# Kernel optimization log

Hardware: AMD Instinct MI355X
Metric: run time of the kernel (lower is better)

Reference implementation:

```python
import jax, jax.numpy as jnp
import numpy as np
import math

B, H, W, Cv, Ct, T = 8, 64, 64, 256, 512, 100
TOP_M = 5
N_PAD = 8  # last N_PAD text tokens are all-zero padding


def _xavier(key, fi, fo):
    lim = math.sqrt(6.0 / (fi + fo))
    return jax.random.uniform(key, (fi, fo), jnp.float32, -lim, lim)


def layernorm(x, g, b, eps=1e-5):
    m = x.mean(-1, keepdims=True)
    v = ((x - m) ** 2).mean(-1, keepdims=True)
    return (x - m) * jax.lax.rsqrt(v + eps) * g + b


def l2norm(x, eps=1e-6):
    n = jnp.sqrt((x * x).sum(-1, keepdims=True))
    return x / jnp.maximum(n, eps)


def setup_inputs() -> dict:
    key = jax.random.key(0)
    ks = jax.random.split(key, 10)
    visual = jax.random.normal(ks[0], (B, H, W, Cv), jnp.float32)
    text = jax.random.normal(ks[1], (B, T, Ct), jnp.float32)
    text = text.at[:, T - N_PAD:, :].set(0.0)  # padded tokens
    return {
        'visual_features': visual,
        'text_features': text,
        'ln1_g': jnp.ones((Cv,), jnp.float32),
        'ln1_b': jnp.zeros((Cv,), jnp.float32),
        'qw': _xavier(ks[2], Cv, Ct), 'qb': jnp.zeros((Ct,), jnp.float32),
        'vw': _xavier(ks[3], Ct, Cv), 'vb': jnp.zeros((Cv,), jnp.float32),
        'gate_w': jax.random.normal(ks[4], (Cv, 1), jnp.float32) * 0.02,
        'gate_b': jnp.zeros((1,), jnp.float32),
        'logit_scale': jnp.asarray(math.log(1.0 / 0.07), jnp.float32),
        'alpha': jnp.asarray(0.1, jnp.float32),
        'ln2_g': jnp.ones((Cv,), jnp.float32),
        'ln2_b': jnp.zeros((Cv,), jnp.float32),
        'w1': jax.random.normal(ks[5], (Cv, 4 * Cv), jnp.float32) * 0.02,
        'b1': jnp.zeros((4 * Cv,), jnp.float32),
        'w2': jax.random.normal(ks[6], (4 * Cv, Cv), jnp.float32) * 0.02,
        'b2': jnp.zeros((Cv,), jnp.float32),
        'top_m': TOP_M,
    }


def reference(visual_features, text_features, ln1_g, ln1_b, qw, qb, vw, vb,
              gate_w, gate_b, logit_scale, alpha, ln2_g, ln2_b, w1, b1, w2, b2,
              top_m):
    Bv, Hh, Ww, C = visual_features.shape
    N = Hh * Ww
    x = layernorm(visual_features, ln1_g, ln1_b).reshape(Bv, N, C)
    q = l2norm(x @ qw + qb)                     # (B,N,Ct)
    k = l2norm(text_features)                   # (B,T,Ct)
    v = text_features @ vw + vb                 # (B,T,Cv)
    pad = jnp.abs(text_features).sum(-1) <= 1e-6  # (B,T) True = padding
    Ctd = float(qw.shape[1])
    scale = jnp.exp(jnp.clip(logit_scale, -2.0, 2.0)) / math.sqrt(Ctd)
    sim = jnp.einsum('bnc,btc->bnt', q, k) * scale
    top_vals, top_idx = jax.lax.top_k(sim, top_m)       # (B,N,M)
    pad_top = jax.vmap(lambda p, i: p[i])(pad, top_idx)  # (B,N,M)
    top_vals = jnp.where(pad_top, -jnp.inf, top_vals)
    attn = jax.nn.softmax(top_vals, axis=-1)
    v_sel = jax.vmap(lambda vb_, ib: vb_[ib])(v, top_idx)  # (B,N,M,Cv)
    aligned = jnp.einsum('bnm,bnmc->bnc', attn, v_sel)
    gate = jax.nn.sigmoid(x @ gate_w + gate_b)  # (B,N,1)
    aligned = aligned * gate
    y = x + alpha * aligned
    y = layernorm(y, ln2_g, ln2_b)
    y = y + (jax.nn.gelu(y @ w1 + b1, approximate=False) @ w2 + b2)
    return y.reshape(Bv, Hh, Ww, C)
```

## Files before the change

kernel.cpp:

```cpp
#include <hip/hip_runtime.h>
#include <hip/hip_bf16.h>
#include <math.h>

using bf16 = __hip_bfloat16;
typedef __attribute__((ext_vector_type(8))) short s16x8;
typedef __attribute__((ext_vector_type(4))) short s16x4;
typedef __attribute__((ext_vector_type(4))) float f32x4;
typedef __attribute__((ext_vector_type(4))) unsigned int u32x4;

static __device__ __forceinline__ float bits2f(unsigned short u) {
  union { unsigned int i; float f; } c; c.i = ((unsigned int)u) << 16; return c.f;
}
static __device__ __forceinline__ unsigned short f2bits(float f) {
  bf16 h = __float2bfloat16(f);
  return *reinterpret_cast<unsigned short*>(&h);
}
static __device__ __forceinline__ unsigned short scrub16(unsigned short u, unsigned short repl) {
  return ((u & 0x7F80u) == 0x7F80u) ? repl : u;
}
static __device__ __forceinline__ unsigned short f2bits_s(float f, unsigned short repl) {
  return scrub16(f2bits(f), repl);
}
static __device__ __forceinline__ float ldf_s(const float* p, float repl) {
  unsigned int w = *reinterpret_cast<const unsigned int*>(p);
  if ((w & 0x7F800000u) == 0x7F800000u) return repl;
  union { unsigned int i; float f; } c; c.i = w; return c.f;
}
static __device__ __forceinline__ float stf_s(float f, float repl) {
  union { float f; unsigned int i; } c; c.f = f;
  if ((c.i & 0x7F800000u) == 0x7F800000u) return repl;
  return f;
}
static __device__ __forceinline__ s16x8 pack8(const float* p) {
  union { f32x4 f; float fe[4]; unsigned int u[4]; } a, b;
  a.f = *reinterpret_cast<const f32x4*>(p);
  b.f = *reinterpret_cast<const f32x4*>(p + 4);
  s16x8 v;
  #pragma unroll
  for (int e = 0; e < 4; e++) {
    const float fa = ((a.u[e] & 0x7F800000u) == 0x7F800000u) ? 0.f : a.fe[e];
    const float fb = ((b.u[e] & 0x7F800000u) == 0x7F800000u) ? 0.f : b.fe[e];
    v[e]     = (short)f2bits_s(fa, 0);
    v[e + 4] = (short)f2bits_s(fb, 0);
  }
  return v;
}
static __device__ __forceinline__ float gelu_fast(float t) {
  const float u = fmaf(0.044715f * t * t, t, t);
  const float e = __expf(-1.5957691216057308f * u);
  return __fdividef(t, 1.f + e);
}
static __device__ __forceinline__ void gload_lds16(const unsigned short* g, unsigned short* l) {
  __builtin_amdgcn_global_load_lds(
      (const __attribute__((address_space(1))) void*)g,
      (__attribute__((address_space(3))) void*)l, 16, 0, 0);
}

static __device__ __forceinline__ float block_sum(float v, float* red, int tid) {
  #pragma unroll
  for (int o = 32; o > 0; o >>= 1) v += __shfl_down(v, o, 64);
  __syncthreads();
  if ((tid & 63) == 0) red[tid >> 6] = v;
  __syncthreads();
  return red[0] + red[1] + red[2] + red[3];
}

__global__ __launch_bounds__(256)
void k_preps(const float* __restrict__ qw, unsigned short* __restrict__ qwt,
             const float* __restrict__ text, unsigned short* __restrict__ khat,
             int* __restrict__ padf,
             const float* __restrict__ w1, const float* __restrict__ w2,
             unsigned short* __restrict__ w1s, unsigned short* __restrict__ w2s,
             int do_ffn,
             const float* __restrict__ vw, const float* __restrict__ vb_,
             float* __restrict__ vf) {
  __shared__ float red[4];
  __shared__ float s_t[512];
  const int bid = blockIdx.x;
  const int tid = threadIdx.x;

  if (bid < 512) {
    const int n = bid, k = tid;
    qwt[n * 256 + (k ^ ((n & 7) << 3))] = f2bits_s(ldf_s(&qw[(long)k * 512 + n], 0.f), 0);
    return;
  }
  if (bid < 1408) {
    const int j = bid - 512;
    const int t = j % 112, b = j / 112;
    unsigned short* kr = khat + ((long)b * 112 + t) * 512;
    if (t >= 100) {
      if (tid < 64) *reinterpret_cast<s16x8*>(&kr[tid * 8]) = (s16x8){0,0,0,0,0,0,0,0};
      return;
    }
    const float* tr = text + ((long)b * 100 + t) * 512;
    const float v0 = ldf_s(&tr[tid], 0.f), v1 = ldf_s(&tr[tid + 256], 0.f);
    const float ss = block_sum(fmaf(v0, v0, v1 * v1), red, tid);
    const float sa = block_sum(fabsf(v0) + fabsf(v1), red, tid);
    const float inv = 1.f / fmaxf(sqrtf(ss), 1e-6f);
    const int ks = tid ^ ((t & 7) << 3);
    kr[ks]       = f2bits_s(v0 * inv, 0);
    kr[ks + 256] = f2bits_s(v1 * inv, 0);
    if (tid == 0) padf[b * 100 + t] = (sa <= 1e-6f) ? 1 : 0;
    return;
  }
  if (bid < 3456) {
    if (!do_ffn) return;
    const int i = (bid - 1408) * 256 + tid;
    if (i < 262144) {
      const int h = i >> 8, k = i & 255;
      w1s[h * 256 + (k ^ ((h & 7) << 3))] = f2bits(w1[(long)k * 1024 + h]);
    } else {
      const int j = i - 262144;
      const int c = j >> 10, h = j & 1023;
      const int hs = (h & ~63) | ((h & 63) ^ ((c & 7) << 3));
      w2s[(long)c * 1024 + hs] = f2bits(w2[(long)h * 256 + c]);
    }
    return;
  }
  {
    const int bt = bid - 3456;
    const float* tr = text + (long)bt * 512;
    s_t[tid]       = ldf_s(&tr[tid], 0.f);
    s_t[tid + 256] = ldf_s(&tr[tid + 256], 0.f);
    __syncthreads();
    float acc = 0.f;
    for (int k = 0; k < 512; k++) acc = fmaf(s_t[k], vw[k * 256 + tid], acc);
    vf[(long)bt * 256 + tid] = stf_s(acc + vb_[tid], 0.f);
  }
}

__global__ __launch_bounds__(512)
void k_simattn(float* xv, const unsigned short* __restrict__ qwt,
               const float* __restrict__ qb, const unsigned short* __restrict__ khat,
               const float* __restrict__ ls, const float* __restrict__ ln1g,
               const float* __restrict__ ln1b, const int* __restrict__ pad,
               const float* __restrict__ v, const float* __restrict__ gate_w,
               const float* __restrict__ gate_b, const float* __restrict__ alpha,
               const float* __restrict__ ln2g, const float* __restrict__ ln2b) {
  __shared__ __align__(16) unsigned short s_q[64][520];
  __shared__ __align__(16) char s_unb[65536];
  __shared__ float s_qn[64];
  unsigned short* s_un = reinterpret_cast<unsigned short*>(s_unb);

  const int tid  = threadIdx.x;
  const int lane = tid & 63;
  const int w    = tid >> 6;
  const int l15  = lane & 15;
  const int lg   = lane >> 4;
  const int b    = blockIdx.y;
  const long grow = (long)b * 4096 + (long)blockIdx.x * 64;

  #pragma unroll
  for (int it = 0; it < 8; it++) {
    const int u = tid + it * 512;
    gload_lds16(&qwt[u * 8], &s_un[u * 8]);
  }

  const int R1 = (w >> 2) * 32;
  s16x8 xa[2][8];
  #pragma unroll
  for (int rb = 0; rb < 2; rb++) {
    float* xr = &xv[(grow + R1 + rb * 16 + l15) * 256 + lg * 8];
    float raw[8][8];
    float sm = 0.f, sq = 0.f;
    #pragma unroll
    for (int ks = 0; ks < 8; ks++) {
      union { f32x4 f; float fe[4]; unsigned int u_[4]; } a, c;
      a.f = *reinterpret_cast<const f32x4*>(xr + ks * 32);
      c.f = *reinterpret_cast<const f32x4*>(xr + ks * 32 + 4);
      #pragma unroll
      for (int e = 0; e < 4; e++) {
        const float va = ((a.u_[e] & 0x7F800000u) == 0x7F800000u) ? 0.f : a.fe[e];
        const float vb = ((c.u_[e] & 0x7F800000u) == 0x7F800000u) ? 0.f : c.fe[e];
        raw[ks][e] = va; raw[ks][e + 4] = vb;
        sm += va + vb;
        sq = fmaf(va, va, sq); sq = fmaf(vb, vb, sq);
      }
    }
    sm += __shfl_xor(sm, 16, 64); sm += __shfl_xor(sm, 32, 64);
    sq += __shfl_xor(sq, 16, 64); sq += __shfl_xor(sq, 32, 64);
    const float mean = sm * (1.f / 256.f);
    const float var  = fmaxf(sq * (1.f / 256.f) - mean * mean, 0.f);
    const float rstd = rsqrtf(var + 1e-5f);
    #pragma unroll
    for (int ks = 0; ks < 8; ks++) {
      const int c0 = ks * 32 + lg * 8;
      const f32x4 g0 = *reinterpret_cast<const f32x4*>(&ln1g[c0]);
      const f32x4 g1 = *reinterpret_cast<const f32x4*>(&ln1g[c0 + 4]);
      const f32x4 bb0 = *reinterpret_cast<const f32x4*>(&ln1b[c0]);
      const f32x4 bb1 = *reinterpret_cast<const f32x4*>(&ln1b[c0 + 4]);
      f32x4 o0, o1; s16x8 vv;
      #pragma unroll
      for (int e = 0; e < 4; e++) {
        const float x0 = stf_s((raw[ks][e] - mean) * rstd * g0[e] + bb0[e], 0.f);
        const float x1 = stf_s((raw[ks][e + 4] - mean) * rstd * g1[e] + bb1[e], 0.f);
        o0[e] = x0; o1[e] = x1;
        vv[e]     = (short)f2bits_s(x0, 0);
        vv[e + 4] = (short)f2bits_s(x1, 0);
      }
      xa[rb][ks] = vv;
      if ((w & 3) == 0) {
        *reinterpret_cast<f32x4*>(xr + ks * 32)     = o0;
        *reinterpret_cast<f32x4*>(xr + ks * 32 + 4) = o1;
      }
    }
  }
  __syncthreads();

  const int C1 = (w & 3) * 32;
  for (int nc = 0; nc < 4; nc++) {
    f32x4 a1[2][2];
    #pragma unroll
    for (int i = 0; i < 2; i++)
      #pragma unroll
      for (int j = 0; j < 2; j++) a1[i][j] = (f32x4){0.f, 0.f, 0.f, 0.f};
    #pragma unroll
    for (int ks = 0; ks < 8; ks++) {
      s16x8 bfr[2];
      #pragma unroll
      for (int cb = 0; cb < 2; cb++) {
        const int nl = C1 + cb * 16 + l15;
        const int byt = nl * 512 + ((ks * 64 + lg * 16) ^ ((nl & 7) << 4));
        bfr[cb] = *reinterpret_cast<const s16x8*>(reinterpret_cast<const char*>(s_un) + byt);
      }
      #pragma unroll
      for (int rb = 0; rb < 2; rb++) {
        a1[rb][0] = __builtin_amdgcn_mfma_f32_16x16x32_bf16(xa[rb][ks], bfr[0], a1[rb][0], 0, 0, 0);
        a1[rb][1] = __builtin_amdgcn_mfma_f32_16x16x32_bf16(xa[rb][ks], bfr[1], a1[rb][1], 0, 0, 0);
      }
    }
    #pragma unroll
    for (int cb = 0; cb < 2; cb++) {
      const int n = nc * 128 + C1 + cb * 16 + l15;
      const float bq = ldf_s(&qb[n], 0.f);
      #pragma unroll
      for (int rb = 0; rb < 2; rb++)
        #pragma unroll
        for (int rg = 0; rg < 4; rg++)
          s_q[R1 + rb * 16 + lg * 4 + rg][n] = f2bits_s(a1[rb][cb][rg] + bq, 0);
    }
    __syncthreads();
    if (nc < 3) {
      const unsigned short* src = qwt + (long)(nc + 1) * 32768;
      #pragma unroll
      for (int it = 0; it < 8; it++) {
        const int u = tid + it * 512;
        gload_lds16(&src[u * 8], &s_un[u * 8]);
      }
      __syncthreads();
    }
  }

  {
    const int r = tid >> 3, ts8 = tid & 7;
    float ss = 0.f;
    #pragma unroll
    for (int j = 0; j < 8; j++) {
      s16x8 vq = *reinterpret_cast<const s16x8*>(&s_q[r][ts8 * 64 + j * 8]);
      #pragma unroll
      for (int e = 0; e < 8; e++) { float f = bits2f((unsigned short)vq[e]); ss = fmaf(f, f, ss); }
    }
    #pragma unroll
    for (int o = 4; o > 0; o >>= 1) ss += __shfl_down(ss, o, 8);
    if (ts8 == 0) s_qn[r] = fmaxf(sqrtf(ss), 1e-6f);
  }

  const int wr = w & 1, wc = w >> 1;
  f32x4 acc[2][2];
  #pragma unroll
  for (int i = 0; i < 2; i++)
    #pragma unroll
    for (int j = 0; j < 2; j++) acc[i][j] = (f32x4){0.f, 0.f, 0.f, 0.f};

  for (int kc = 0; kc < 2; kc++) {
    #pragma unroll
    for (int it = 0; it < 7; it++) {
      const int u = it * 512 + tid;
      const int t = u >> 5, kb = (u & 31) * 8;
      gload_lds16(&khat[((long)b * 112 + t) * 512 + kc * 256 + kb], &s_un[u * 8]);
    }
    __syncthreads();
    #pragma unroll
    for (int ks = 0; ks < 8; ks++) {
      const int ko = kc * 256 + ks * 32 + lg * 8;
      s16x8 af[2], bfr[2];
      #pragma unroll
      for (int rb = 0; rb < 2; rb++)
        af[rb] = *reinterpret_cast<const s16x8*>(&s_q[(2 * wr + rb) * 16 + l15][ko]);
      #pragma unroll
      for (int cb = 0; cb < 2; cb++)
        if (2 * wc + cb < 7) {
          const int t = (2 * wc + cb) * 16 + l15;
          bfr[cb] = *reinterpret_cast<const s16x8*>(
              &s_un[t * 256 + ((ks * 32 + lg * 8) ^ ((t & 7) << 3))]);
        }
      #pragma unroll
      for (int rb = 0; rb < 2; rb++)
        #pragma unroll
        for (int cb = 0; cb < 2; cb++)
          if (2 * wc + cb < 7)
            acc[rb][cb] = __builtin_amdgcn_mfma_f32_16x16x32_bf16(af[rb], bfr[cb], acc[rb][cb], 0, 0, 0);
    }
    __syncthreads();
  }

  float (*s_x)[260]    = reinterpret_cast<float(*)[260]>(&s_q[0][0]);
  float (*s_simf)[116] = reinterpret_cast<float(*)[116]>(s_unb);
  float (*s_attn)[8]   = reinterpret_cast<float(*)[8]>(s_unb + 32768);
  int   (*s_idx)[8]    = reinterpret_cast<int(*)[8]>(s_unb + 34816);
  float* s_gate = reinterpret_cast<float*>(s_unb + 36864);
  float* s_mu   = reinterpret_cast<float*>(s_unb + 37120);
  float* s_rs   = reinterpret_cast<float*>(s_unb + 37376);
  int*   s_pad  = reinterpret_cast<int*>(s_unb + 37632);

  {
    float l = ldf_s(&ls[0], 0.f);
    l = fminf(fmaxf(l, -2.f), 2.f);
    const float scale = expf(l) * 0.04419417382415922f;
    #pragma unroll
    for (int rb = 0; rb < 2; rb++)
      #pragma unroll
      for (int rg = 0; rg < 4; rg++) {
        const int row = (2 * wr + rb) * 16 + lg * 4 + rg;
        const float inv = scale / s_qn[row];
        #pragma unroll
        for (int cb = 0; cb < 2; cb++) {
          if (2 * wc + cb < 7) {
            const int tcol = (2 * wc + cb) * 16 + l15;
            s_simf[row][tcol] = acc[rb][cb][rg] * inv;
          }
        }
      }
  }
  #pragma unroll
  for (int it = 0; it < 8; it++) {
    const int u = tid + it * 512;
    const int row = u >> 6, c4 = (u & 63) * 4;
    union { f32x4 f; float fe[4]; unsigned int w_[4]; } cc;
    cc.f = *reinterpret_cast<const f32x4*>(&xv[(grow + row) * 256 + c4]);
    #pragma unroll
    for (int e = 0; e < 4; e++)
      if ((cc.w_[e] & 0x7F800000u) == 0x7F800000u) cc.fe[e] = 0.f;
    *reinterpret_cast<f32x4*>(&s_x[row][c4]) = cc.f;
  }
  if (tid < 112) s_pad[tid] = (tid < 100) ? pad[b * 100 + tid] : 1;
  __syncthreads();

  const int r = tid >> 3, ts = tid & 7;
  float loc[14];
  #pragma unroll
  for (int j = 0; j < 14; j++) {
    int t = ts * 14 + j;
    loc[j] = (t < 100) ? s_simf[r][t] : -1e38f;
  }
  float topv[5]; int topi[5];
  for (int it = 0; it < 5; it++) {
    float bv = -1e38f; int bi = 1 << 20;
    #pragma unroll
    for (int j = 0; j < 14; j++) {
      if (loc[j] > bv) { bv = loc[j]; bi = ts * 14 + j; }
    }
    #pragma unroll
    for (int o = 4; o > 0; o >>= 1) {
      float ov = __shfl_down(bv, o, 8);
      int   oi = __shfl_down(bi, o, 8);
      if (ov > bv || (ov == bv && oi < bi)) { bv = ov; bi = oi; }
    }
    bv = __shfl(bv, 0, 8); bi = __shfl(bi, 0, 8);
    const int bic = (bi < 0) ? 0 : (bi > 99 ? 99 : bi);
    topv[it] = bv; topi[it] = bic;
    const int rel = bi - ts * 14;
    if (rel >= 0 && rel < 14) loc[rel] = -1e38f;
  }
  {
    float tv[5], mx = -1e38f;
    #pragma unroll
    for (int m = 0; m < 5; m++) { tv[m] = s_pad[topi[m]] ? -1e38f : topv[m]; mx = fmaxf(mx, tv[m]); }
    const float mxs = (mx > -1e37f) ? mx : 0.f;
    float se = 0.f, ev[5];
    #pragma unroll
    for (int m = 0; m < 5; m++) {
      ev[m] = (tv[m] > -1e37f) ? expf(fminf(tv[m] - mxs, 0.f)) : 0.f;
      se += ev[m];
    }
    const float rse = (se > 0.f) ? 1.f / se : 0.f;
    if (ts == 0) {
      #pragma unroll
      for (int m = 0; m < 5; m++) { s_attn[r][m] = ev[m] * rse; s_idx[r][m] = topi[m]; }
    }
  }
  {
    float gd = 0.f;
    #pragma unroll
    for (int j = 0; j < 32; j++) {
      int c = ts + 8 * j;
      gd = fmaf(s_x[r][c], gate_w[c], gd);
    }
    #pragma unroll
    for (int o = 4; o > 0; o >>= 1) gd += __shfl_down(gd, o, 8);
    if (ts == 0) s_gate[r] = 1.f / (1.f + expf(fminf(-(gd + gate_b[0]), 80.f)));
  }
  __syncthreads();
  const float al = alpha[0];
  const float* vb_ = v + (long)b * 100 * 256;
  #pragma unroll
  for (int it = 0; it < 8; it++) {
    const int u = tid + it * 512;
    const int row = u >> 6, c4 = (u & 63) * 4;
    f32x4 acc4 = (f32x4){0.f, 0.f, 0.f, 0.f};
    #pragma unroll
    for (int m = 0; m < 5; m++) {
      const float am = s_attn[row][m];
      union { f32x4 f; float fe[4]; unsigned int w_[4]; } vv;
      vv.f = *reinterpret_cast<const f32x4*>(&vb_[(long)s_idx[row][m] * 256 + c4]);
      #pragma unroll
      for (int e = 0; e < 4; e++) {
        const float fv = ((vv.w_[e] & 0x7F800000u) == 0x7F800000u) ? 0.f : vv.fe[e];
        acc4[e] = fmaf(am, fv, acc4[e]);
      }
    }
    const float gr_ = s_gate[row];
    f32x4 xq = *reinterpret_cast<f32x4*>(&s_x[row][c4]);
    #pragma unroll
    for (int e = 0; e < 4; e++) xq[e] = xq[e] + al * (acc4[e] * gr_);
    *reinterpret_cast<f32x4*>(&s_x[row][c4]) = xq;
  }
  __syncthreads();
  {
    float sm = 0.f;
    #pragma unroll
    for (int j = 0; j < 32; j++) sm += s_x[r][ts + 8 * j];
    #pragma unroll
    for (int o = 4; o > 0; o >>= 1) sm += __shfl_down(sm, o, 8);
    sm = __shfl(sm, 0, 8);
    const float mean = sm * (1.f / 256.f);
    float vr = 0.f;
    #pragma unroll
    for (int j = 0; j < 32; j++) { float d = s_x[r][ts + 8 * j] - mean; vr = fmaf(d, d, vr); }
    #pragma unroll
    for (int o = 4; o > 0; o >>= 1) vr += __shfl_down(vr, o, 8);
    if (ts == 0) { s_mu[r] = mean; s_rs[r] = rsqrtf(vr * (1.f / 256.f) + 1e-5f); }
  }
  __syncthreads();
  #pragma unroll
  for (int it = 0; it < 8; it++) {
    const int u = tid + it * 512;
    const int row = u >> 6, c4 = (u & 63) * 4;
    f32x4 yv;
    #pragma unroll
    for (int e = 0; e < 4; e++) {
      const int c = c4 + e;
      yv[e] = stf_s((s_x[row][c] - s_mu[row]) * s_rs[row] * ln2g[c] + ln2b[c], 100.0f);
    }
    *reinterpret_cast<f32x4*>(&xv[(grow + row) * 256 + c4]) = yv;
  }
}

__global__ __launch_bounds__(512, 4)
void k_ffn_mfma(const float* __restrict__ yln,
                const unsigned short* __restrict__ w1s,
                const float* __restrict__ b1,
                const unsigned short* __restrict__ w2s,
                const float* __restrict__ b2,
                float* __restrict__ out) {
  __shared__ __align__(16) unsigned short s_w1[64 * 256];
  __shared__ __align__(16) unsigned short s_w2[256 * 64];
  __shared__ __align__(16) unsigned short s_h[64 * 64];

  const int tid  = threadIdx.x;
  const int lane = tid & 63;
  const int w    = tid >> 6;
  const int l15  = lane & 15;
  const int lg   = lane >> 4;
  const long gr0 = (long)blockIdx.x * 64;

  #pragma unroll
  for (int it = 0; it < 4; it++) {
    const int u = tid + it * 512;
    gload_lds16(&w1s[u * 8], &s_w1[u * 8]);
  }

  const int R1 = (w >> 1) * 16, C1 = (w & 1) * 32;
  const int R0 = (w >> 2) * 32, C0 = (w & 3) * 64;

  s16x8 ya[8];
  {
    const float* xr = &yln[(gr0 + R1 + l15) * 256];
    #pragma unroll
    for (int ks = 0; ks < 8; ks++)
      ya[ks] = pack8(xr + ks * 32 + lg * 8);
  }

  f32x4 acc[2][4];
  #pragma unroll
  for (int i = 0; i < 2; i++)
    #pragma unroll
    for (int j = 0; j < 4; j++)
      acc[i][j] = (f32x4){0.f, 0.f, 0.f, 0.f};

  __syncthreads();

  for (int kc = 0; kc < 16; kc++) {
    const int hc = kc * 64;
    #pragma unroll
    for (int it = 0; it < 4; it++) {
      const int u = tid + it * 512;
      const int c = u >> 3, k8 = (u & 7) * 8;
      gload_lds16(&w2s[(long)c * 1024 + hc + k8], &s_w2[u * 8]);
    }

    f32x4 a1[2];
    a1[0] = (f32x4){0.f, 0.f, 0.f, 0.f};
    a1[1] = (f32x4){0.f, 0.f, 0.f, 0.f};
    __builtin_amdgcn_s_setprio(1);
    #pragma unroll
    for (int ks = 0; ks < 8; ks++) {
      const int ko = ks * 32 + lg * 8;
      const int n0_ = C1 + l15, n1_ = C1 + 16 + l15;
      const s16x8 bf0 = *reinterpret_cast<const s16x8*>(&s_w1[n0_ * 256 + (ko ^ ((n0_ & 7) << 3))]);
      const s16x8 bf1 = *reinterpret_cast<const s16x8*>(&s_w1[n1_ * 256 + (ko ^ ((n1_ & 7) << 3))]);
      a1[0] = __builtin_amdgcn_mfma_f32_16x16x32_bf16(ya[ks], bf0, a1[0], 0, 0, 0);
      a1[1] = __builtin_amdgcn_mfma_f32_16x16x32_bf16(ya[ks], bf1, a1[1], 0, 0, 0);
    }
    __builtin_amdgcn_s_setprio(0);
    #pragma unroll
    for (int cb = 0; cb < 2; cb++) {
      const int col = C1 + cb * 16 + l15;
      const float bb = b1[hc + col];
      #pragma unroll
      for (int rg = 0; rg < 4; rg++) {
        const int row = R1 + lg * 4 + rg;
        const float t = a1[cb][rg] + bb;
        s_h[row * 64 + (col ^ ((row & 7) << 3))] = f2bits_s(gelu_fast(t), 0);
      }
    }
    __syncthreads();

    if (kc < 15) {
      #pragma unroll
      for (int it = 0; it < 4; it++) {
        const int u = tid + it * 512;
        gload_lds16(&w1s[(long)(hc + 64) * 256 + u * 8], &s_w1[u * 8]);
      }
    }

    __builtin_amdgcn_s_setprio(1);
    #pragma unroll
    for (int p = 0; p < 2; p++) {
      const int ko = p * 32 + lg * 8;
      s16x8 bfr[4];
      #pragma unroll
      for (int cb = 0; cb < 4; cb++) {
        const int c = C0 + cb * 16 + l15;
        bfr[cb] = *reinterpret_cast<const s16x8*>(&s_w2[c * 64 + (ko ^ ((c & 7) << 3))]);
      }
      #pragma unroll
      for (int rb = 0; rb < 2; rb++) {
        const int hr = R0 + rb * 16 + l15;
        const s16x8 af = *reinterpret_cast<const s16x8*>(&s_h[hr * 64 + (ko ^ ((hr & 7) << 3))]);
        #pragma unroll
        for (int cb = 0; cb < 4; cb++)
          acc[rb][cb] = __builtin_amdgcn_mfma_f32_16x16x32_bf16(af, bfr[cb], acc[rb][cb], 0, 0, 0);
      }
    }
    __builtin_amdgcn_s_setprio(0);
    __syncthreads();
  }

  #pragma unroll
  for (int rb = 0; rb < 2; rb++)
    #pragma unroll
    for (int rg = 0; rg < 4; rg++) {
      const int R = R0 + rb * 16 + lg * 4 + rg;
      const float* yr = &yln[(gr0 + R) * 256];
      #pragma unroll
      for (int cb = 0; cb < 4; cb++) {
        const int C = C0 + cb * 16 + l15;
        out[(gr0 + R) * 256 + C] =
            stf_s(ldf_s(&yr[C], 0.f) + acc[rb][cb][rg] + b2[C], 300.0f);
      }
    }
}

#define FR 32
__global__ __launch_bounds__(256)
void k_ffn(const float* __restrict__ yln, const float* __restrict__ w1,
           const float* __restrict__ b1, const float* __restrict__ w2,
           const float* __restrict__ b2, float* __restrict__ out) {
  __shared__ unsigned short s_y[FR][256];
  __shared__ float s_h[FR][66];
  __shared__ unsigned short s_w[64 * 256];
  const int tid = threadIdx.x;
  const long gr0 = (long)blockIdx.x * FR;
  for (int i = tid; i < FR * 256; i += 256)
    (&s_y[0][0])[i] = f2bits_s(ldf_s(&yln[gr0 * 256 + i], 0.f), 0);
  const int ty = tid >> 4, tx = tid & 15;
  const int r = tid >> 3, ts = tid & 7;
  float acc[32];
  #pragma unroll
  for (int j = 0; j < 32; j++) acc[j] = 0.f;
  for (int kc = 0; kc < 16; kc++) {
    __syncthreads();
    for (int i = tid; i < 64 * 256; i += 256) {
      int kk = i >> 6, c = i & 63;
      s_w[i] = f2bits(w1[(long)kk * 1024 + kc * 64 + c]);
    }
    __syncthreads();
    {
      float a2[2][4] = {{0.f,0.f,0.f,0.f},{0.f,0.f,0.f,0.f}};
      for (int k = 0; k < 256; k++) {
        const float a0 = bits2f(s_y[ty * 2][k]);
        const float a1 = bits2f(s_y[ty * 2 + 1][k]);
        #pragma unroll
        for (int j = 0; j < 4; j++) {
          const float bv = bits2f(s_w[k * 64 + tx * 4 + j]);
          a2[0][j] = fmaf(a0, bv, a2[0][j]);
          a2[1][j] = fmaf(a1, bv, a2[1][j]);
        }
      }
      #pragma unroll
      for (int i = 0; i < 2; i++)
        #pragma unroll
        for (int j = 0; j < 4; j++) {
          float t = a2[i][j] + b1[kc * 64 + tx * 4 + j];
          s_h[ty * 2 + i][tx * 4 + j] = 0.5f * t * (1.f + erff(t * 0.7071067811865475f));
        }
    }
    __syncthreads();
    for (int i = tid; i < 64 * 256; i += 256) {
      int kk = i >> 8, c = i & 255;
      s_w[i] = f2bits(w2[(long)(kc * 64 + kk) * 256 + c]);
    }
    __syncthreads();
    for (int kk = 0; kk < 64; kk++) {
      const float hv = s_h[r][kk];
      #pragma unroll
      for (int jj = 0; jj < 8; jj++) {
        #pragma unroll
        for (int u = 0; u < 4; u++) {
          const float wv = bits2f(s_w[kk * 256 + ts * 4 + 32 * jj + u]);
          acc[jj * 4 + u] = fmaf(hv, wv, acc[jj * 4 + u]);
        }
      }
    }
  }
  #pragma unroll
  for (int jj = 0; jj < 8; jj++) {
    #pragma unroll
    for (int u = 0; u < 4; u++) {
      int c = ts * 4 + 32 * jj + u;
      out[(gr0 + r) * 256 + c] = stf_s(bits2f(s_y[r][c]) + acc[jj * 4 + u] + b2[c], 300.0f);
    }
  }
}

__global__ __launch_bounds__(256)
void k_fill(float* __restrict__ out, long n, float V) {
  long i = (long)blockIdx.x * 256 + threadIdx.x;
  if (i < n) out[i] = V;
}

extern "C" void kernel_launch(void* const* d_in, const int* in_sizes, int n_in,
                              void* d_out, int out_size, void* d_ws, size_t ws_size,
                              hipStream_t stream) {
  static const int DEXP[19] = {8388608,409600,256,256,131072,512,131072,256,256,1,
                               1,1,256,256,262144,1024,262144,256,1};
  static const int S19[19] = {15,12,6,5,11,10,16,14,4,3,9,0,8,7,17,1,18,2,13};
  static const int S18[18] = {14,12,6,5,11,10,15,13,4,3,9,0,8,7,16,1,17,2};
  static const int ID19[19] = {0,1,2,3,4,5,6,7,8,9,10,11,12,13,14,15,16,17,18};

  auto okmap = [&](const int* P, int cnt, int need_n) -> bool {
    if (n_in != need_n) return false;
    for (int i = 0; i < cnt; i++)
      if (in_sizes[P[i]] != DEXP[i]) return false;
    return true;
  };

  const int* M = nullptr;
  if      (okmap(S19, 19, 19)) M = S19;
  else if (okmap(S18, 18, 18)) M = S18;
  else if (okmap(ID19, 19, 19) || okmap(ID19, 18, 18)) M = ID19;

  if (!M) {
    float V;
    if (n_in == 19 || n_in == 18) {
      int bad = 0;
      while (bad < n_in && bad < 19 && in_sizes[bad] == DEXP[bad]) bad++;
      V = 1024.f * (float)(1 + bad);
    } else {
      V = 32.f * (float)n_in + 16.f;
    }
    long n = (long)out_size;
    k_fill<<<(int)((n + 255) / 256), 256, 0, stream>>>((float*)d_out, n, V);
    return;
  }

  float*       vis  = (float*)d_in[M[0]];
  const float* text = (const float*)d_in[M[1]];
  const float* ln1g = (const float*)d_in[M[2]];
  const float* ln1b = (const float*)d_in[M[3]];
  const float* qw   = (const float*)d_in[M[4]];
  const float* qb   = (const float*)d_in[M[5]];
  const float* vw   = (const float*)d_in[M[6]];
  const float* vb   = (const float*)d_in[M[7]];
  const float* gw   = (const float*)d_in[M[8]];
  const float* gb   = (const float*)d_in[M[9]];
  const float* ls   = (const float*)d_in[M[10]];
  const float* alp  = (const float*)d_in[M[11]];
  const float* ln2g = (const float*)d_in[M[12]];
  const float* ln2b = (const float*)d_in[M[13]];
  const float* w1   = (const float*)d_in[M[14]];
  const float* b1   = (const float*)d_in[M[15]];
  const float* w2   = (const float*)d_in[M[16]];
  const float* b2   = (const float*)d_in[M[17]];

  float* vf   = (float*)d_out;
  int*   padf = (int*)  ((char*)d_out + 819200);
  unsigned short* qwt  = (unsigned short*)((char*)d_out + 822400);
  unsigned short* khat = (unsigned short*)((char*)d_out + 1346688);
  float* outp = (float*)d_out;

  const bool mfma_ffn = (d_ws != nullptr) && (ws_size >= (size_t)1048576);
  unsigned short* w1s = (unsigned short*)d_ws;
  unsigned short* w2s = w1s + 262144;

  k_preps<<<4256, 256, 0, stream>>>(qw, qwt, text, khat, padf,
                                    w1, w2, w1s, w2s, mfma_ffn ? 1 : 0,
                                    vw, vb, vf);
  k_simattn<<<dim3(64, 8), 512, 0, stream>>>(vis, qwt, qb, khat, ls, ln1g, ln1b,
                                             padf, vf, gw, gb, alp, ln2g, ln2b);
  if (mfma_ffn)
    k_ffn_mfma<<<512, 512, 0, stream>>>(vis, w1s, b1, w2s, b2, outp);
  else
    k_ffn <<<1024, 256, 0, stream>>>(vis, w1, b1, w2, b2, outp);
}
```

Measured before the change: 289.0 us.

## Halve simattn tile to 32 rows and transpose weights through LDS tiles

The similarity/attention kernel now handles 32 pixel rows per block instead of 64. It launches twice as many blocks, with half the shared memory per block and launch bounds requesting 4 waves per SIMD, to raise occupancy. Every MFMA loop, reduction width and LDS offset is reworked to match the smaller tile. Separately, the weight transpose/cast prep now uses 64-row LDS-staged tiles with vectorized 16-byte stores instead of one scalar strided element per thread, which cuts the prep grid size. The costs are that each block re-stages the full qwt matrix for fewer rows, and there is more per-block overhead.

```diff
diff --git a/kernel.cpp b/kernel.cpp
--- a/kernel.cpp
+++ b/kernel.cpp
@@ -74,18 +74,71 @@
              int do_ffn,
              const float* __restrict__ vw, const float* __restrict__ vb_,
              float* __restrict__ vf) {
+  __shared__ __align__(16) unsigned short t16[64 * 256];
   __shared__ float red[4];
   __shared__ float s_t[512];
   const int bid = blockIdx.x;
   const int tid = threadIdx.x;
 
-  if (bid < 512) {
-    const int n = bid, k = tid;
-    qwt[n * 256 + (k ^ ((n & 7) << 3))] = f2bits_s(ldf_s(&qw[(long)k * 512 + n], 0.f), 0);
+  if (bid < 8) {
+    const int n0 = bid * 64;
+    const int nl = tid & 63;
+    for (int p = 0; p < 64; p++) {
+      const int k = p * 4 + (tid >> 6);
+      t16[nl * 256 + (k ^ ((nl & 7) << 3))] =
+          f2bits_s(ldf_s(&qw[(long)k * 512 + n0 + nl], 0.f), 0);
+    }
+    __syncthreads();
+    #pragma unroll
+    for (int p = 0; p < 8; p++) {
+      const int u = p * 256 + tid;
+      const int r = u >> 5, k8 = (u & 31) * 8;
+      *reinterpret_cast<s16x8*>(&qwt[(long)(n0 + r) * 256 + k8]) =
+          *reinterpret_cast<const s16x8*>(&t16[r * 256 + k8]);
+    }
     return;
   }
-  if (bid < 1408) {
-    const int j = bid - 512;
+  if (bid < 24) {
+    if (!do_ffn) return;
+    const int h0 = (bid - 8) * 64;
+    const int hl = tid & 63;
+    for (int p = 0; p < 64; p++) {
+      const int k = p * 4 + (tid >> 6);
+      t16[hl * 256 + (k ^ ((hl & 7) << 3))] =
+          f2bits(w1[(long)k * 1024 + h0 + hl]);
+    }
+    __syncthreads();
+    #pragma unroll
+    for (int p = 0; p < 8; p++) {
+      const int u = p * 256 + tid;
+      const int r = u >> 5, k8 = (u & 31) * 8;
+      *reinterpret_cast<s16x8*>(&w1s[(long)(h0 + r) * 256 + k8]) =
+          *reinterpret_cast<const s16x8*>(&t16[r * 256 + k8]);
+    }
+    return;
+  }
+  if (bid < 40) {
+    if (!do_ffn) return;
+    const int j = bid - 24;
+    const int c0 = (j & 3) * 64, h0 = (j >> 2) * 256;
+    const int cl = tid & 63;
+    for (int p = 0; p < 64; p++) {
+      const int hh = p * 4 + (tid >> 6);
+      const int hs = (hh & ~63) | ((hh & 63) ^ ((cl & 7) << 3));
+      t16[cl * 256 + hs] = f2bits(w2[(long)(h0 + hh) * 256 + c0 + cl]);
+    }
+    __syncthreads();
+    #pragma unroll
+    for (int p = 0; p < 8; p++) {
+      const int u = p * 256 + tid;
+      const int r = u >> 5, h8 = (u & 31) * 8;
+      *reinterpret_cast<s16x8*>(&w2s[(long)(c0 + r) * 1024 + h0 + h8]) =
+          *reinterpret_cast<const s16x8*>(&t16[r * 256 + h8]);
+    }
+    return;
+  }
+  if (bid < 936) {
+    const int j = bid - 40;
     const int t = j % 112, b = j / 112;
     unsigned short* kr = khat + ((long)b * 112 + t) * 512;
     if (t >= 100) {
@@ -103,22 +156,8 @@
     if (tid == 0) padf[b * 100 + t] = (sa <= 1e-6f) ? 1 : 0;
     return;
   }
-  if (bid < 3456) {
-    if (!do_ffn) return;
-    const int i = (bid - 1408) * 256 + tid;
-    if (i < 262144) {
-      const int h = i >> 8, k = i & 255;
-      w1s[h * 256 + (k ^ ((h & 7) << 3))] = f2bits(w1[(long)k * 1024 + h]);
-    } else {
-      const int j = i - 262144;
-      const int c = j >> 10, h = j & 1023;
-      const int hs = (h & ~63) | ((h & 63) ^ ((c & 7) << 3));
-      w2s[(long)c * 1024 + hs] = f2bits(w2[(long)h * 256 + c]);
-    }
-    return;
-  }
   {
-    const int bt = bid - 3456;
+    const int bt = bid - 936;
     const float* tr = text + (long)bt * 512;
     s_t[tid]       = ldf_s(&tr[tid], 0.f);
     s_t[tid + 256] = ldf_s(&tr[tid + 256], 0.f);
@@ -129,7 +168,7 @@
   }
 }
 
-__global__ __launch_bounds__(512)
+__global__ __launch_bounds__(512, 4)
 void k_simattn(float* xv, const unsigned short* __restrict__ qwt,
                const float* __restrict__ qb, const unsigned short* __restrict__ khat,
                const float* __restrict__ ls, const float* __restrict__ ln1g,
@@ -137,9 +176,9 @@
                const float* __restrict__ v, const float* __restrict__ gate_w,
                const float* __restrict__ gate_b, const float* __restrict__ alpha,
                const float* __restrict__ ln2g, const float* __restrict__ ln2b) {
-  __shared__ __align__(16) unsigned short s_q[64][520];
-  __shared__ __align__(16) char s_unb[65536];
-  __shared__ float s_qn[64];
+  __shared__ __align__(16) unsigned short s_q[32][520];
+  __shared__ __align__(16) char s_unb[32768];
+  __shared__ float s_qn[32];
   unsigned short* s_un = reinterpret_cast<unsigned short*>(s_unb);
 
   const int tid  = threadIdx.x;
@@ -148,19 +187,18 @@
   const int l15  = lane & 15;
   const int lg   = lane >> 4;
   const int b    = blockIdx.y;
-  const long grow = (long)b * 4096 + (long)blockIdx.x * 64;
-
-  #pragma unroll
-  for (int it = 0; it < 8; it++) {
+  const long grow = (long)b * 4096 + (long)blockIdx.x * 32;
+
+  #pragma unroll
+  for (int it = 0; it < 4; it++) {
     const int u = tid + it * 512;
     gload_lds16(&qwt[u * 8], &s_un[u * 8]);
   }
 
-  const int R1 = (w >> 2) * 32;
-  s16x8 xa[2][8];
-  #pragma unroll
-  for (int rb = 0; rb < 2; rb++) {
-    float* xr = &xv[(grow + R1 + rb * 16 + l15) * 256 + lg * 8];
+  const int R1 = (w >> 2) * 16;
+  s16x8 xa[8];
+  {
+    float* xr = &xv[(grow + R1 + l15) * 256 + lg * 8];
     float raw[8][8];
     float sm = 0.f, sq = 0.f;
     #pragma unroll
@@ -198,7 +236,7 @@
         vv[e]     = (short)f2bits_s(x0, 0);
         vv[e + 4] = (short)f2bits_s(x1, 0);
       }
-      xa[rb][ks] = vv;
+      xa[ks] = vv;
       if ((w & 3) == 0) {
         *reinterpret_cast<f32x4*>(xr + ks * 32)     = o0;
         *reinterpret_cast<f32x4*>(xr + ks * 32 + 4) = o1;
@@ -207,43 +245,28 @@
   }
   __syncthreads();
 
-  const int C1 = (w & 3) * 32;
-  for (int nc = 0; nc < 4; nc++) {
-    f32x4 a1[2][2];
-    #pragma unroll
-    for (int i = 0; i < 2; i++)
-      #pragma unroll
-      for (int j = 0; j < 2; j++) a1[i][j] = (f32x4){0.f, 0.f, 0.f, 0.f};
+  const int C1 = (w & 3) * 16;
+  for (int nc = 0; nc < 8; nc++) {
+    f32x4 a1 = (f32x4){0.f, 0.f, 0.f, 0.f};
     #pragma unroll
     for (int ks = 0; ks < 8; ks++) {
-      s16x8 bfr[2];
-      #pragma unroll
-      for (int cb = 0; cb < 2; cb++) {
-        const int nl = C1 + cb * 16 + l15;
-        const int byt = nl * 512 + ((ks * 64 + lg * 16) ^ ((nl & 7) << 4));
-        bfr[cb] = *reinterpret_cast<const s16x8*>(reinterpret_cast<const char*>(s_un) + byt);
-      }
-      #pragma unroll
-      for (int rb = 0; rb < 2; rb++) {
-        a1[rb][0] = __builtin_amdgcn_mfma_f32_16x16x32_bf16(xa[rb][ks], bfr[0], a1[rb][0], 0, 0, 0);
-        a1[rb][1] = __builtin_amdgcn_mfma_f32_16x16x32_bf16(xa[rb][ks], bfr[1], a1[rb][1], 0, 0, 0);
-      }
-    }
-    #pragma unroll
-    for (int cb = 0; cb < 2; cb++) {
-      const int n = nc * 128 + C1 + cb * 16 + l15;
+      const int nl = C1 + l15;
+      const s16x8 bf = *reinterpret_cast<const s16x8*>(
+          &s_un[nl * 256 + ((ks * 32 + lg * 8) ^ ((nl & 7) << 3))]);
+      a1 = __builtin_amdgcn_mfma_f32_16x16x32_bf16(xa[ks], bf, a1, 0, 0, 0);
+    }
+    {
+      const int n = nc * 64 + C1 + l15;
       const float bq = ldf_s(&qb[n], 0.f);
       #pragma unroll
-      for (int rb = 0; rb < 2; rb++)
-        #pragma unroll
-        for (int rg = 0; rg < 4; rg++)
-          s_q[R1 + rb * 16 + lg * 4 + rg][n] = f2bits_s(a1[rb][cb][rg] + bq, 0);
-    }
-    __syncthreads();
-    if (nc < 3) {
-      const unsigned short* src = qwt + (long)(nc + 1) * 32768;
-      #pragma unroll
-      for (int it = 0; it < 8; it++) {
+      for (int rg = 0; rg < 4; rg++)
+        s_q[R1 + lg * 4 + rg][n] = f2bits_s(a1[rg] + bq, 0);
+    }
+    __syncthreads();
+    if (nc < 7) {
+      const unsigned short* src = qwt + (long)(nc + 1) * 16384;
+      #pragma unroll
+      for (int it = 0; it < 4; it++) {
         const int u = tid + it * 512;
         gload_lds16(&src[u * 8], &s_un[u * 8]);
       }
@@ -252,88 +275,78 @@
   }
 
   {
-    const int r = tid >> 3, ts8 = tid & 7;
+    const int rq = tid >> 4, tq = tid & 15;
     float ss = 0.f;
     #pragma unroll
-    for (int j = 0; j < 8; j++) {
-      s16x8 vq = *reinterpret_cast<const s16x8*>(&s_q[r][ts8 * 64 + j * 8]);
+    for (int j = 0; j < 4; j++) {
+      s16x8 vq = *reinterpret_cast<const s16x8*>(&s_q[rq][tq * 32 + j * 8]);
       #pragma unroll
       for (int e = 0; e < 8; e++) { float f = bits2f((unsigned short)vq[e]); ss = fmaf(f, f, ss); }
     }
     #pragma unroll
-    for (int o = 4; o > 0; o >>= 1) ss += __shfl_down(ss, o, 8);
-    if (ts8 == 0) s_qn[r] = fmaxf(sqrtf(ss), 1e-6f);
+    for (int o = 8; o > 0; o >>= 1) ss += __shfl_down(ss, o, 16);
+    if (tq == 0) s_qn[rq] = fmaxf(sqrtf(ss), 1e-6f);
   }
 
   const int wr = w & 1, wc = w >> 1;
-  f32x4 acc[2][2];
-  #pragma unroll
-  for (int i = 0; i < 2; i++)
-    #pragma unroll
-    for (int j = 0; j < 2; j++) acc[i][j] = (f32x4){0.f, 0.f, 0.f, 0.f};
-
-  for (int kc = 0; kc < 2; kc++) {
-    #pragma unroll
-    for (int it = 0; it < 7; it++) {
+  f32x4 acc[2];
+  acc[0] = (f32x4){0.f, 0.f, 0.f, 0.f};
+  acc[1] = (f32x4){0.f, 0.f, 0.f, 0.f};
+
+  for (int kc = 0; kc < 4; kc++) {
+    #pragma unroll
+    for (int it = 0; it < 4; it++) {
       const int u = it * 512 + tid;
-      const int t = u >> 5, kb = (u & 31) * 8;
-      gload_lds16(&khat[((long)b * 112 + t) * 512 + kc * 256 + kb], &s_un[u * 8]);
-    }
-    __syncthreads();
-    #pragma unroll
-    for (int ks = 0; ks < 8; ks++) {
-      const int ko = kc * 256 + ks * 32 + lg * 8;
-      s16x8 af[2], bfr[2];
-      #pragma unroll
-      for (int rb = 0; rb < 2; rb++)
-        af[rb] = *reinterpret_cast<const s16x8*>(&s_q[(2 * wr + rb) * 16 + l15][ko]);
-      #pragma unroll
-      for (int cb = 0; cb < 2; cb++)
-        if (2 * wc + cb < 7) {
-          const int t = (2 * wc + cb) * 16 + l15;
-          bfr[cb] = *reinterpret_cast<const s16x8*>(
-              &s_un[t * 256 + ((ks * 32 + lg * 8) ^ ((t & 7) << 3))]);
+      if (u < 1792) {
+        const int t = u >> 4, kb = (u & 15) * 8;
+        gload_lds16(&khat[((long)b * 112 + t) * 512 + kc * 128 + kb], &s_un[u * 8]);
+      }
+    }
+    __syncthreads();
+    #pragma unroll
+    for (int ks = 0; ks < 4; ks++) {
+      const int ko = kc * 128 + ks * 32 + lg * 8;
+      const s16x8 af = *reinterpret_cast<const s16x8*>(&s_q[wr * 16 + l15][ko]);
+      #pragma unroll
+      for (int cb = 0; cb < 2; cb++) {
+        const int ct = wc * 2 + cb;
+        if (ct < 7) {
+          const int t = ct * 16 + l15;
+          const s16x8 bf = *reinterpret_cast<const s16x8*>(
+              &s_un[t * 128 + ((ks * 32 + lg * 8) ^ ((t & 7) << 3))]);
+          acc[cb] = __builtin_amdgcn_mfma_f32_16x16x32_bf16(af, bf, acc[cb], 0, 0, 0);
         }
-      #pragma unroll
-      for (int rb = 0; rb < 2; rb++)
-        #pragma unroll
-        for (int cb = 0; cb < 2; cb++)
-          if (2 * wc + cb < 7)
-            acc[rb][cb] = __builtin_amdgcn_mfma_f32_16x16x32_bf16(af[rb], bfr[cb], acc[rb][cb], 0, 0, 0);
+      }
     }
     __syncthreads();
   }
 
   float (*s_x)[260]    = reinterpret_cast<float(*)[260]>(&s_q[0][0]);
   float (*s_simf)[116] = reinterpret_cast<float(*)[116]>(s_unb);
-  float (*s_attn)[8]   = reinterpret_cast<float(*)[8]>(s_unb + 32768);
-  int   (*s_idx)[8]    = reinterpret_cast<int(*)[8]>(s_unb + 34816);
-  float* s_gate = reinterpret_cast<float*>(s_unb + 36864);
-  float* s_mu   = reinterpret_cast<float*>(s_unb + 37120);
-  float* s_rs   = reinterpret_cast<float*>(s_unb + 37376);
-  int*   s_pad  = reinterpret_cast<int*>(s_unb + 37632);
+  float (*s_attn)[8]   = reinterpret_cast<float(*)[8]>(s_unb + 16384);
+  int   (*s_idx)[8]    = reinterpret_cast<int(*)[8]>(s_unb + 17408);
+  float* s_gate = reinterpret_cast<float*>(s_unb + 18432);
+  float* s_mu   = reinterpret_cast<float*>(s_unb + 18560);
+  float* s_rs   = reinterpret_cast<float*>(s_unb + 18688);
+  int*   s_pad  = reinterpret_cast<int*>(s_unb + 18816);
 
   {
     float l = ldf_s(&ls[0], 0.f);
     l = fminf(fmaxf(l, -2.f), 2.f);
     const float scale = expf(l) * 0.04419417382415922f;
     #pragma unroll
-    for (int rb = 0; rb < 2; rb++)
-      #pragma unroll
-      for (int rg = 0; rg < 4; rg++) {
-        const int row = (2 * wr + rb) * 16 + lg * 4 + rg;
-        const float inv = scale / s_qn[row];
-        #pragma unroll
-        for (int cb = 0; cb < 2; cb++) {
-          if (2 * wc + cb < 7) {
-            const int tcol = (2 * wc + cb) * 16 + l15;
-            s_simf[row][tcol] = acc[rb][cb][rg] * inv;
-          }
-        }
-      }
-  }
-  #pragma unroll
-  for (int it = 0; it < 8; it++) {
+    for (int rg = 0; rg < 4; rg++) {
+      const int row = wr * 16 + lg * 4 + rg;
+      const float inv = scale / s_qn[row];
+      #pragma unroll
+      for (int cb = 0; cb < 2; cb++) {
+        const int ct = wc * 2 + cb;
+        if (ct < 7) s_simf[row][ct * 16 + l15] = acc[cb][rg] * inv;
+      }
+    }
+  }
+  #pragma unroll
+  for (int it = 0; it < 4; it++) {
     const int u = tid + it * 512;
     const int row = u >> 6, c4 = (u & 63) * 4;
     union { f32x4 f; float fe[4]; unsigned int w_[4]; } cc;
@@ -346,31 +359,31 @@
   if (tid < 112) s_pad[tid] = (tid < 100) ? pad[b * 100 + tid] : 1;
   __syncthreads();
 
-  const int r = tid >> 3, ts = tid & 7;
-  float loc[14];
-  #pragma unroll
-  for (int j = 0; j < 14; j++) {
-    int t = ts * 14 + j;
+  const int r = tid >> 4, ts = tid & 15;
+  float loc[7];
+  #pragma unroll
+  for (int j = 0; j < 7; j++) {
+    int t = ts * 7 + j;
     loc[j] = (t < 100) ? s_simf[r][t] : -1e38f;
   }
   float topv[5]; int topi[5];
   for (int it = 0; it < 5; it++) {
     float bv = -1e38f; int bi = 1 << 20;
     #pragma unroll
-    for (int j = 0; j < 14; j++) {
-      if (loc[j] > bv) { bv = loc[j]; bi = ts * 14 + j; }
-    }
-    #pragma unroll
-    for (int o = 4; o > 0; o >>= 1) {
-      float ov = __shfl_down(bv, o, 8);
-      int   oi = __shfl_down(bi, o, 8);
+    for (int j = 0; j < 7; j++) {
+      if (loc[j] > bv) { bv = loc[j]; bi = ts * 7 + j; }
+    }
+    #pragma unroll
+    for (int o = 8; o > 0; o >>= 1) {
+      float ov = __shfl_down(bv, o, 16);
+      int   oi = __shfl_down(bi, o, 16);
       if (ov > bv || (ov == bv && oi < bi)) { bv = ov; bi = oi; }
     }
-    bv = __shfl(bv, 0, 8); bi = __shfl(bi, 0, 8);
+    bv = __shfl(bv, 0, 16); bi = __shfl(bi, 0, 16);
     const int bic = (bi < 0) ? 0 : (bi > 99 ? 99 : bi);
     topv[it] = bv; topi[it] = bic;
-    const int rel = bi - ts * 14;
-    if (rel >= 0 && rel < 14) loc[rel] = -1e38f;
+    const int rel = bi - ts * 7;
+    if (rel >= 0 && rel < 7) loc[rel] = -1e38f;
   }
   {
     float tv[5], mx = -1e38f;
@@ -392,19 +405,19 @@
   {
     float gd = 0.f;
     #pragma unroll
-    for (int j = 0; j < 32; j++) {
-      int c = ts + 8 * j;
+    for (int j = 0; j < 16; j++) {
+      int c = ts + 16 * j;
       gd = fmaf(s_x[r][c], gate_w[c], gd);
     }
     #pragma unroll
-    for (int o = 4; o > 0; o >>= 1) gd += __shfl_down(gd, o, 8);
+    for (int o = 8; o > 0; o >>= 1) gd += __shfl_down(gd, o, 16);
     if (ts == 0) s_gate[r] = 1.f / (1.f + expf(fminf(-(gd + gate_b[0]), 80.f)));
   }
   __syncthreads();
   const float al = alpha[0];
   const float* vb_ = v + (long)b * 100 * 256;
   #pragma unroll
-  for (int it = 0; it < 8; it++) {
+  for (int it = 0; it < 4; it++) {
     const int u = tid + it * 512;
     const int row = u >> 6, c4 = (u & 63) * 4;
     f32x4 acc4 = (f32x4){0.f, 0.f, 0.f, 0.f};
@@ -429,21 +442,21 @@
   {
     float sm = 0.f;
     #pragma unroll
-    for (int j = 0; j < 32; j++) sm += s_x[r][ts + 8 * j];
-    #pragma unroll
-    for (int o = 4; o > 0; o >>= 1) sm += __shfl_down(sm, o, 8);
-    sm = __shfl(sm, 0, 8);
+    for (int j = 0; j < 16; j++) sm += s_x[r][ts + 16 * j];
+    #pragma unroll
+    for (int o = 8; o > 0; o >>= 1) sm += __shfl_down(sm, o, 16);
+    sm = __shfl(sm, 0, 16);
     const float mean = sm * (1.f / 256.f);
     float vr = 0.f;
     #pragma unroll
-    for (int j = 0; j < 32; j++) { float d = s_x[r][ts + 8 * j] - mean; vr = fmaf(d, d, vr); }
-    #pragma unroll
-    for (int o = 4; o > 0; o >>= 1) vr += __shfl_down(vr, o, 8);
+    for (int j = 0; j < 16; j++) { float d = s_x[r][ts + 16 * j] - mean; vr = fmaf(d, d, vr); }
+    #pragma unroll
+    for (int o = 8; o > 0; o >>= 1) vr += __shfl_down(vr, o, 16);
     if (ts == 0) { s_mu[r] = mean; s_rs[r] = rsqrtf(vr * (1.f / 256.f) + 1e-5f); }
   }
   __syncthreads();
   #pragma unroll
-  for (int it = 0; it < 8; it++) {
+  for (int it = 0; it < 4; it++) {
     const int u = tid + it * 512;
     const int row = u >> 6, c4 = (u & 63) * 4;
     f32x4 yv;
@@ -724,11 +737,11 @@
   unsigned short* w1s = (unsigned short*)d_ws;
   unsigned short* w2s = w1s + 262144;
 
-  k_preps<<<4256, 256, 0, stream>>>(qw, qwt, text, khat, padf,
+  k_preps<<<1736, 256, 0, stream>>>(qw, qwt, text, khat, padf,
                                     w1, w2, w1s, w2s, mfma_ffn ? 1 : 0,
                                     vw, vb, vf);
-  k_simattn<<<dim3(64, 8), 512, 0, stream>>>(vis, qwt, qb, khat, ls, ln1g, ln1b,
-                                             padf, vf, gw, gb, alp, ln2g, ln2b);
+  k_simattn<<<dim3(128, 8), 512, 0, stream>>>(vis, qwt, qb, khat, ls, ln1g, ln1b,
+                                              padf, vf, gw, gb, alp, ln2g, ln2b);
   if (mfma_ffn)
     k_ffn_mfma<<<512, 512, 0, stream>>>(vis, w1s, b1, w2s, b2, outp);
   else
```

Measured after the change: 263.4 us. -8.8%, faster.
